# Kernel tuning notes

Hardware: AMD Instinct MI355X
Metric: run time of the kernel (lower is better)

## Reference

```python
import jax, jax.numpy as jnp
import numpy as np

B, T, D = 32, 2048, 512
BATCH_SIZE = 32  # config.batch_size: number of MVN draws


def setup_inputs() -> dict:
    key = jax.random.key(0)
    k1, k2 = jax.random.split(key)
    x = jax.random.normal(k1, (B, T, D), dtype=jnp.float32)
    z = jax.random.normal(k2, (BATCH_SIZE, D), dtype=jnp.float32)  # standard-normal noise for reparameterized MVN draw
    return {"x": x, "z": z}


def reference(x, z):
    # mean over batch and time -> [D]
    mean = jnp.mean(x, axis=(0, 1))
    # per-batch covariance over time axis, then mean over batch -> [D, D]
    t = x.shape[1]
    xc = x - jnp.mean(x, axis=1, keepdims=True)
    # sum over b and t fused: equals mean_b( xc_b^T xc_b / (t-1) )
    cov = jnp.einsum('btd,bte->de', xc, xc) / ((t - 1) * x.shape[0])
    # multivariate normal draw via Cholesky reparameterization:
    # sample = mean + z @ L^T, L L^T = cov
    L = jnp.linalg.cholesky(cov)
    return mean + z @ L.T
```

## Files before the change

kernel.cpp:

```cpp
#include <hip/hip_runtime.h>

#define Dn 512
#define Bn 32
#define Tn 2048
#define BT 65536

typedef unsigned short u16;
typedef __attribute__((ext_vector_type(8))) short short8;
typedef __attribute__((ext_vector_type(4))) float floatx4;

__device__ __forceinline__ u16 f2bf(float f) {
    unsigned u = __float_as_uint(f);
    unsigned r = (u + 0x7FFFu + ((u >> 16) & 1u)) >> 16;
    return (u16)r;
}
__device__ __forceinline__ float bf2f(u16 s) { return __uint_as_float(((unsigned)s) << 16); }

#define REP64(X) X(0) X(1) X(2) X(3) X(4) X(5) X(6) X(7) X(8) X(9) X(10) X(11) X(12) X(13) X(14) X(15) \
    X(16) X(17) X(18) X(19) X(20) X(21) X(22) X(23) X(24) X(25) X(26) X(27) X(28) X(29) X(30) X(31) \
    X(32) X(33) X(34) X(35) X(36) X(37) X(38) X(39) X(40) X(41) X(42) X(43) X(44) X(45) X(46) X(47) \
    X(48) X(49) X(50) X(51) X(52) X(53) X(54) X(55) X(56) X(57) X(58) X(59) X(60) X(61) X(62) X(63)
#define REPJ(OP, K) OP(K,0) OP(K,1) OP(K,2) OP(K,3) OP(K,4) OP(K,5) OP(K,6) OP(K,7) OP(K,8) OP(K,9) \
    OP(K,10) OP(K,11) OP(K,12) OP(K,13) OP(K,14) OP(K,15) OP(K,16) OP(K,17) OP(K,18) OP(K,19) \
    OP(K,20) OP(K,21) OP(K,22) OP(K,23) OP(K,24) OP(K,25) OP(K,26) OP(K,27) OP(K,28) OP(K,29) \
    OP(K,30) OP(K,31) OP(K,32) OP(K,33) OP(K,34) OP(K,35) OP(K,36) OP(K,37) OP(K,38) OP(K,39) \
    OP(K,40) OP(K,41) OP(K,42) OP(K,43) OP(K,44) OP(K,45) OP(K,46) OP(K,47) OP(K,48) OP(K,49) \
    OP(K,50) OP(K,51) OP(K,52) OP(K,53) OP(K,54) OP(K,55) OP(K,56) OP(K,57) OP(K,58) OP(K,59) \
    OP(K,60) OP(K,61) OP(K,62) OP(K,63)
#define REPQ(OP, C) OP(C,0,0,0) OP(C,1,0,1) OP(C,2,0,2) OP(C,3,0,3) OP(C,4,1,0) OP(C,5,1,1) OP(C,6,1,2) OP(C,7,1,3) \
    OP(C,8,2,0) OP(C,9,2,1) OP(C,10,2,2) OP(C,11,2,3) OP(C,12,3,0) OP(C,13,3,1) OP(C,14,3,2) OP(C,15,3,3) \
    OP(C,16,4,0) OP(C,17,4,1) OP(C,18,4,2) OP(C,19,4,3) OP(C,20,5,0) OP(C,21,5,1) OP(C,22,5,2) OP(C,23,5,3) \
    OP(C,24,6,0) OP(C,25,6,1) OP(C,26,6,2) OP(C,27,6,3) OP(C,28,7,0) OP(C,29,7,1) OP(C,30,7,2) OP(C,31,7,3) \
    OP(C,32,8,0) OP(C,33,8,1) OP(C,34,8,2) OP(C,35,8,3) OP(C,36,9,0) OP(C,37,9,1) OP(C,38,9,2) OP(C,39,9,3) \
    OP(C,40,10,0) OP(C,41,10,1) OP(C,42,10,2) OP(C,43,10,3) OP(C,44,11,0) OP(C,45,11,1) OP(C,46,11,2) OP(C,47,11,3) \
    OP(C,48,12,0) OP(C,49,12,1) OP(C,50,12,2) OP(C,51,12,3) OP(C,52,13,0) OP(C,53,13,1) OP(C,54,13,2) OP(C,55,13,3) \
    OP(C,56,14,0) OP(C,57,14,1) OP(C,58,14,2) OP(C,59,14,3) OP(C,60,15,0) OP(C,61,15,1) OP(C,62,15,2) OP(C,63,15,3)
#define REPW(OP) OP(0,0,1,2,3) OP(1,4,5,6,7) OP(2,8,9,10,11) OP(3,12,13,14,15) OP(4,16,17,18,19) \
    OP(5,20,21,22,23) OP(6,24,25,26,27) OP(7,28,29,30,31) OP(8,32,33,34,35) OP(9,36,37,38,39) \
    OP(10,40,41,42,43) OP(11,44,45,46,47) OP(12,48,49,50,51) OP(13,52,53,54,55) OP(14,56,57,58,59) \
    OP(15,60,61,62,63)
#define REP16C(OP, C) OP(C,0) OP(C,1) OP(C,2) OP(C,3) OP(C,4) OP(C,5) OP(C,6) OP(C,7) \
    OP(C,8) OP(C,9) OP(C,10) OP(C,11) OP(C,12) OP(C,13) OP(C,14) OP(C,15)

__global__ __launch_bounds__(256) void k_transpose(const float* __restrict__ x,
                                                   u16* __restrict__ Xt) {
    int tt = blockIdx.x;
    int dt = blockIdx.y;
    int b  = blockIdx.z;
    __shared__ u16 sT[64][68];
    int tid = threadIdx.x;
    int row = tid >> 4;
    int c4  = (tid & 15) * 4;
    const float* src = x + ((long)b * Tn + (long)tt * 64) * Dn + dt * 64;
#pragma unroll
    for (int q = 0; q < 4; q++) {
        int r = row + q * 16;
        floatx4 v = *(const floatx4*)(src + (long)r * Dn + c4);
        sT[c4 + 0][r] = f2bf(v[0]);
        sT[c4 + 1][r] = f2bf(v[1]);
        sT[c4 + 2][r] = f2bf(v[2]);
        sT[c4 + 3][r] = f2bf(v[3]);
    }
    __syncthreads();
    int drow = tid >> 3;
    int koff = (tid & 7) * 8;
    long kout = (long)b * Tn + (long)tt * 64 + koff;
#pragma unroll
    for (int p = 0; p < 2; p++) {
        int dr = drow + p * 32;
        u16 tmp[8];
#pragma unroll
        for (int j = 0; j < 8; j++) tmp[j] = sT[dr][koff + j];
        *(short8*)(Xt + (long)(dt * 64 + dr) * BT + kout) = *(short8*)tmp;
    }
}

__global__ __launch_bounds__(256) void k_mu(const u16* __restrict__ Xt,
                                            float* __restrict__ mu) {
    int tid = threadIdx.x;
    int wave = tid >> 6, lane = tid & 63;
    int p = blockIdx.x * 4 + wave;
    int b = p >> 9, d = p & 511;
    const u16* src = Xt + (long)d * BT + (long)b * Tn;
    float s = 0.f;
#pragma unroll
    for (int c = 0; c < 4; c++) {
        short8 v = *(const short8*)(src + c * 512 + lane * 8);
#pragma unroll
        for (int j = 0; j < 8; j++) s += bf2f((u16)v[j]);
    }
#pragma unroll
    for (int off = 32; off; off >>= 1) s += __shfl_down(s, off, 64);
    if (lane == 0) mu[p] = s * (1.0f / Tn);
}

#define LDK 40
__global__ __launch_bounds__(256) void k_gram(const u16* __restrict__ Xt,
                                              float* __restrict__ partial) {
    int chunk = blockIdx.x;
    int pos = blockIdx.y;
    int di = (pos < 4) ? 0 : (pos < 7) ? 1 : (pos < 9) ? 2 : 3;
    int start = di * 4 - (di * (di - 1)) / 2;
    int ei = di + (pos - start);
    int d0 = di * 128, e0 = ei * 128;

    __shared__ u16 sA[128 * LDK];
    __shared__ u16 sB[128 * LDK];
    int tid = threadIdx.x;
    int wave = tid >> 6, lane = tid & 63;
    int wm = wave & 1, wn = wave >> 1;
    int lrow = tid >> 2;
    int lk = (tid & 3) * 8;
    const u16* gA = Xt + (long)(d0 + lrow) * BT + (long)chunk * 4096 + lk;
    const u16* gB = Xt + (long)(e0 + lrow) * BT + (long)chunk * 4096 + lk;
    int m = lane & 15, g = lane >> 4;

    floatx4 acc[4][4] = {};
    for (int kk = 0; kk < 4096; kk += 32) {
        short8 a0 = *(const short8*)(gA + kk);
        short8 a1 = *(const short8*)(gA + 64l * BT + kk);
        short8 b0 = *(const short8*)(gB + kk);
        short8 b1 = *(const short8*)(gB + 64l * BT + kk);
        __syncthreads();
        *(short8*)(sA + lrow * LDK + lk) = a0;
        *(short8*)(sA + (lrow + 64) * LDK + lk) = a1;
        *(short8*)(sB + lrow * LDK + lk) = b0;
        *(short8*)(sB + (lrow + 64) * LDK + lk) = b1;
        __syncthreads();
        short8 af[4], bf[4];
#pragma unroll
        for (int i = 0; i < 4; i++)
            af[i] = *(const short8*)(sA + (wm * 64 + i * 16 + m) * LDK + g * 8);
#pragma unroll
        for (int j = 0; j < 4; j++)
            bf[j] = *(const short8*)(sB + (wn * 64 + j * 16 + m) * LDK + g * 8);
#pragma unroll
        for (int i = 0; i < 4; i++)
#pragma unroll
            for (int j = 0; j < 4; j++)
                acc[i][j] = __builtin_amdgcn_mfma_f32_16x16x32_bf16(af[i], bf[j], acc[i][j], 0, 0, 0);
    }
    float* P = partial + (long)chunk * (512l * 512);
    int col = lane & 15, rowg = (lane >> 4) * 4;
#pragma unroll
    for (int i = 0; i < 4; i++)
#pragma unroll
        for (int j = 0; j < 4; j++) {
            int rr = d0 + wm * 64 + i * 16 + rowg;
            int cc = e0 + wn * 64 + j * 16 + col;
#pragma unroll
            for (int r = 0; r < 4; r++) P[(long)(rr + r) * 512 + cc] = acc[i][j][r];
        }
}

__global__ __launch_bounds__(256) void k_assemble(const float* __restrict__ partial,
                                                  const float* __restrict__ mu,
                                                  float* __restrict__ A) {
    int d = blockIdx.y;
    int e = blockIdx.x * 256 + threadIdx.x;
    int bd = d >> 7, be = e >> 7;
    long idx = (bd <= be) ? ((long)d * 512 + e) : ((long)e * 512 + d);
    float s = 0.f;
#pragma unroll
    for (int c = 0; c < 16; c++) s += partial[c * (512l * 512) + idx];
    float msum = 0.f;
#pragma unroll
    for (int b = 0; b < 32; b++) msum += mu[b * 512 + d] * mu[b * 512 + e];
    A[(long)d * 512 + e] = (s - (float)Tn * msum) * (1.0f / ((Tn - 1.0f) * Bn));
}

__global__ __launch_bounds__(64, 1) void k_chol_panel(float* __restrict__ A, int kb) {
    const int k0 = kb * 64;
    const int lane = threadIdx.x;
    __shared__ float sD[64 * 68];
    __shared__ float sInv[64];
    const floatx4 z4 = {0.f, 0.f, 0.f, 0.f};

    const float* Dr = A + (long)(k0 + lane) * 512 + k0;
#define LDV(Q,A0,A1,A2,A3) floatx4 v##Q = *(const floatx4*)(Dr + 4*(Q));
    REPW(LDV)
#undef LDV
#define DECR(C,M,Mq,e) float r##M = v##Mq[(e)];
    REPQ(DECR, 0)
#undef DECR

    float vinv = 0.f;
#define SH1(K,J) float t##J = ((J) > (K)) ? __shfl(lik, (J), 64) : 0.0f;
#define FM1(K,J) if ((J) > (K)) r##J = fmaf(-lik, t##J, r##J);
#define STEP(K) { float akk = __shfl(r##K, (K), 64); float sd = sqrtf(akk); \
                  float inv = 1.0f / sd; float lik = (lane == (K)) ? sd : r##K * inv; \
                  r##K = lik; if (lane == (K)) vinv = inv; REPJ(SH1, K) REPJ(FM1, K) }
    REP64(STEP)
#undef STEP
#undef FM1
#undef SH1

    if (blockIdx.x == 0) {
        float* W = A + (long)(k0 + lane) * 512 + k0;
#define STW(Q,A0,A1,A2,A3) { floatx4 w; w[0]=r##A0; w[1]=r##A1; w[2]=r##A2; w[3]=r##A3; \
                             *(floatx4*)(W + 4*(Q)) = w; }
        REPW(STW)
#undef STW
        return;
    }

#define STD(Q,A0,A1,A2,A3) { floatx4 w; w[0]=r##A0; w[1]=r##A1; w[2]=r##A2; w[3]=r##A3; \
                             *(floatx4*)(sD + lane * 68 + 4*(Q)) = w; }
    REPW(STD)
#undef STD
    sInv[lane] = vinv;
    __syncthreads();

    int rbase = k0 + 64 + (blockIdx.x - 1) * 64;
    const float* R = A + (long)(rbase + lane) * 512 + k0;
#define LDA(Q,A0,A1,A2,A3) floatx4 u##Q = *(const floatx4*)(R + 4*(Q));
    REPW(LDA)
#undef LDA
#define DECA(C,M,Mq,e) float a##M = u##Mq[(e)];
    REPQ(DECA, 0)
#undef DECA
#define LQ(C,Q) floatx4 q##Q = ((C) > 4*(Q)) ? *(const floatx4*)(sD + (C) * 68 + 4*(Q)) : z4;
#define TF(C,M,Mq,e) if ((M) < (C)) acc##e = fmaf(a##M, q##Mq[(e)], acc##e);
#define TSTEP(C) { REP16C(LQ, C) float acc0 = 0.f, acc1 = 0.f, acc2 = 0.f, acc3 = 0.f; \
                   REPQ(TF, C) a##C = (a##C - ((acc0 + acc1) + (acc2 + acc3))) * sInv[(C)]; }
    REP64(TSTEP)
#undef TSTEP
#undef TF
#undef LQ

    float* Wr = A + (long)(rbase + lane) * 512 + k0;
#define STA(Q,A0,A1,A2,A3) { floatx4 w; w[0]=a##A0; w[1]=a##A1; w[2]=a##A2; w[3]=a##A3; \
                             *(floatx4*)(Wr + 4*(Q)) = w; }
    REPW(STA)
#undef STA
}

__global__ __launch_bounds__(256) void k_chol_update(float* __restrict__ A, int kb) {
    int k0 = kb * 64, base = k0 + 64;
    int idx = blockIdx.x, ti = 0;
    while (idx > ti) { idx -= ti + 1; ti++; }
    int tj = idx;
    int r0 = base + ti * 64, c0 = base + tj * 64;
    __shared__ float sI[64][65];
    __shared__ float sJ[64][65];
    int tid = threadIdx.x;
    int row = tid >> 4, c4 = (tid & 15) * 4;
#pragma unroll
    for (int q = 0; q < 4; q++) {
        int rr = row + q * 16;
        *(floatx4*)&sI[rr][c4] = *(const floatx4*)(A + (long)(r0 + rr) * 512 + k0 + c4);
        *(floatx4*)&sJ[rr][c4] = *(const floatx4*)(A + (long)(c0 + rr) * 512 + k0 + c4);
    }
    __syncthreads();
    int ri = (tid >> 4) * 4, cj = (tid & 15) * 4;
    float acc[4][4] = {};
    for (int k = 0; k < 64; k += 4) {
        floatx4 av[4], bv[4];
#pragma unroll
        for (int ii = 0; ii < 4; ii++) av[ii] = *(const floatx4*)&sI[ri + ii][k];
#pragma unroll
        for (int jj = 0; jj < 4; jj++) bv[jj] = *(const floatx4*)&sJ[cj + jj][k];
#pragma unroll
        for (int ii = 0; ii < 4; ii++)
#pragma unroll
            for (int jj = 0; jj < 4; jj++)
#pragma unroll
                for (int q = 0; q < 4; q++)
                    acc[ii][jj] = fmaf(av[ii][q], bv[jj][q], acc[ii][jj]);
    }
#pragma unroll
    for (int ii = 0; ii < 4; ii++) {
        float* dst = A + (long)(r0 + ri + ii) * 512 + c0 + cj;
        floatx4 old = *(const floatx4*)dst;
#pragma unroll
        for (int jj = 0; jj < 4; jj++) old[jj] -= acc[ii][jj];
        *(floatx4*)dst = old;
    }
}

__global__ __launch_bounds__(512) void k_output(const float* __restrict__ z,
                                                const float* __restrict__ A,
                                                const float* __restrict__ mu,
                                                float* __restrict__ out) {
    int i = blockIdx.x, d = threadIdx.x;
    __shared__ float sz[512];
    sz[d] = z[(long)i * 512 + d];
    __syncthreads();
    float mean = 0.f;
#pragma unroll
    for (int b = 0; b < 32; b++) mean += mu[b * 512 + d];
    mean *= (1.0f / 32.0f);
    const float* Lr = A + (long)d * 512;
    float acc = 0.f;
    int dmax = d + 1;
    int e4 = dmax & ~3;
    for (int e = 0; e < e4; e += 4) {
        floatx4 l = *(const floatx4*)(Lr + e);
        acc += l[0] * sz[e] + l[1] * sz[e + 1] + l[2] * sz[e + 2] + l[3] * sz[e + 3];
    }
    for (int e = e4; e < dmax; e++) acc += Lr[e] * sz[e];
    out[(long)i * 512 + d] = mean + acc;
}

extern "C" void kernel_launch(void* const* d_in, const int* in_sizes, int n_in,
                              void* d_out, int out_size, void* d_ws, size_t ws_size,
                              hipStream_t stream) {
    const float* x = (const float*)d_in[0];
    const float* z = (const float*)d_in[1];
    float* out = (float*)d_out;
    char* ws = (char*)d_ws;
    u16* Xt = (u16*)ws;
    float* mu = (float*)(ws + 67108864);
    float* partial = (float*)(ws + 67108864 + 65536);
    float* A = (float*)(ws + 67108864 + 65536 + 16777216);

    k_transpose<<<dim3(32, 8, 32), 256, 0, stream>>>(x, Xt);
    k_mu<<<4096, 256, 0, stream>>>(Xt, mu);
    k_gram<<<dim3(16, 10), 256, 0, stream>>>(Xt, partial);
    k_assemble<<<dim3(2, 512), 256, 0, stream>>>(partial, mu, A);
    for (int kb = 0; kb < 8; kb++) {
        int nb = 7 - kb;
        k_chol_panel<<<nb + 1, 64, 0, stream>>>(A, kb);
        int tiles = nb * (nb + 1) / 2;
        if (tiles > 0) k_chol_update<<<tiles, 256, 0, stream>>>(A, kb);
    }
    k_output<<<32, 512, 0, stream>>>(z, A, mu, out);
}
```

Before: 674.0 us.

## Split Gram into more chunks with direct LDS loads; switch Cholesky to left-looking

The Gram kernel now splits the time axis into 64 chunks instead of 16, giving 640 blocks rather than 160, and stages tiles with global_load_lds into unpadded shared memory. The assemble kernel sums 64 partials accordingly, and the partial buffer grows fourfold. The Cholesky is restructured from right-looking (a panel kernel plus a trailing-update kernel per step) into one left-looking kernel per step, which halves the number of launches. That kernel accumulates prior updates for its diagonal and sub-diagonal block before factorising. This trades redundant recomputation of the diagonal update in every block, plus extra partial-sum traffic, for better GPU occupancy and less launch overhead.

```diff
diff --git a/kernel.cpp b/kernel.cpp
--- a/kernel.cpp
+++ b/kernel.cpp
@@ -15,6 +15,10 @@
     return (u16)r;
 }
 __device__ __forceinline__ float bf2f(u16 s) { return __uint_as_float(((unsigned)s) << 16); }
+
+#define GLD16(gp, lp) __builtin_amdgcn_global_load_lds( \
+    (const __attribute__((address_space(1))) unsigned int*)(gp), \
+    (__attribute__((address_space(3))) unsigned int*)(lp), 16, 0, 0)
 
 #define REP64(X) X(0) X(1) X(2) X(3) X(4) X(5) X(6) X(7) X(8) X(9) X(10) X(11) X(12) X(13) X(14) X(15) \
     X(16) X(17) X(18) X(19) X(20) X(21) X(22) X(23) X(24) X(25) X(26) X(27) X(28) X(29) X(30) X(31) \
@@ -94,7 +98,6 @@
     if (lane == 0) mu[p] = s * (1.0f / Tn);
 }
 
-#define LDK 40
 __global__ __launch_bounds__(256) void k_gram(const u16* __restrict__ Xt,
                                               float* __restrict__ partial) {
     int chunk = blockIdx.x;
@@ -103,37 +106,35 @@
     int start = di * 4 - (di * (di - 1)) / 2;
     int ei = di + (pos - start);
     int d0 = di * 128, e0 = ei * 128;
-
-    __shared__ u16 sA[128 * LDK];
-    __shared__ u16 sB[128 * LDK];
+    long cb = (long)chunk << 10;
+
+    __shared__ u16 sA[128 * 32];
+    __shared__ u16 sB[128 * 32];
     int tid = threadIdx.x;
     int wave = tid >> 6, lane = tid & 63;
     int wm = wave & 1, wn = wave >> 1;
-    int lrow = tid >> 2;
-    int lk = (tid & 3) * 8;
-    const u16* gA = Xt + (long)(d0 + lrow) * BT + (long)chunk * 4096 + lk;
-    const u16* gB = Xt + (long)(e0 + lrow) * BT + (long)chunk * 4096 + lk;
     int m = lane & 15, g = lane >> 4;
 
+    const u16* gA0 = Xt + (long)(d0 + wave * 32 + (lane >> 2)) * BT + cb + (lane & 3) * 8;
+    const u16* gB0 = Xt + (long)(e0 + wave * 32 + (lane >> 2)) * BT + cb + (lane & 3) * 8;
+    u16* lA = sA + wave * 1024;
+    u16* lB = sB + wave * 1024;
+
     floatx4 acc[4][4] = {};
-    for (int kk = 0; kk < 4096; kk += 32) {
-        short8 a0 = *(const short8*)(gA + kk);
-        short8 a1 = *(const short8*)(gA + 64l * BT + kk);
-        short8 b0 = *(const short8*)(gB + kk);
-        short8 b1 = *(const short8*)(gB + 64l * BT + kk);
+    for (int kk = 0; kk < 1024; kk += 32) {
         __syncthreads();
-        *(short8*)(sA + lrow * LDK + lk) = a0;
-        *(short8*)(sA + (lrow + 64) * LDK + lk) = a1;
-        *(short8*)(sB + lrow * LDK + lk) = b0;
-        *(short8*)(sB + (lrow + 64) * LDK + lk) = b1;
+        GLD16(gA0 + kk, lA);
+        GLD16(gA0 + 16l * BT + kk, lA + 512);
+        GLD16(gB0 + kk, lB);
+        GLD16(gB0 + 16l * BT + kk, lB + 512);
         __syncthreads();
         short8 af[4], bf[4];
 #pragma unroll
         for (int i = 0; i < 4; i++)
-            af[i] = *(const short8*)(sA + (wm * 64 + i * 16 + m) * LDK + g * 8);
+            af[i] = *(const short8*)(sA + (wm * 64 + i * 16 + m) * 32 + g * 8);
 #pragma unroll
         for (int j = 0; j < 4; j++)
-            bf[j] = *(const short8*)(sB + (wn * 64 + j * 16 + m) * LDK + g * 8);
+            bf[j] = *(const short8*)(sB + (wn * 64 + j * 16 + m) * 32 + g * 8);
 #pragma unroll
         for (int i = 0; i < 4; i++)
 #pragma unroll
@@ -161,120 +162,129 @@
     int bd = d >> 7, be = e >> 7;
     long idx = (bd <= be) ? ((long)d * 512 + e) : ((long)e * 512 + d);
     float s = 0.f;
-#pragma unroll
-    for (int c = 0; c < 16; c++) s += partial[c * (512l * 512) + idx];
+#pragma unroll 8
+    for (int c = 0; c < 64; c++) s += partial[c * (512l * 512) + idx];
     float msum = 0.f;
 #pragma unroll
     for (int b = 0; b < 32; b++) msum += mu[b * 512 + d] * mu[b * 512 + e];
     A[(long)d * 512 + e] = (s - (float)Tn * msum) * (1.0f / ((Tn - 1.0f) * Bn));
 }
 
-__global__ __launch_bounds__(64, 1) void k_chol_panel(float* __restrict__ A, int kb) {
+__global__ __launch_bounds__(256, 1) void k_chol_left(float* __restrict__ A, int kb) {
     const int k0 = kb * 64;
-    const int lane = threadIdx.x;
+    const int bi = blockIdx.x;
+    const int r0 = k0 + bi * 64;
+    const int tid = threadIdx.x;
+    const int lane = tid & 63;
+    const int wv = tid >> 6;
+    __shared__ float sLd[64 * 65];
+    __shared__ float sLr[64 * 65];
     __shared__ float sD[64 * 68];
+    __shared__ float sS[64 * 68];
     __shared__ float sInv[64];
     const floatx4 z4 = {0.f, 0.f, 0.f, 0.f};
 
-    const float* Dr = A + (long)(k0 + lane) * 512 + k0;
+    int srow = tid >> 4, c4 = (tid & 15) * 4;
+    int ri = (tid >> 4) * 4, cj = (tid & 15) * 4;
+
+    floatx4 accD[4], accS[4];
+#pragma unroll
+    for (int ii = 0; ii < 4; ii++) {
+        accD[ii] = *(const floatx4*)(A + (long)(k0 + ri + ii) * 512 + k0 + cj);
+        accS[ii] = *(const floatx4*)(A + (long)(r0 + ri + ii) * 512 + k0 + cj);
+    }
+
+    for (int kc = 0; kc < k0; kc += 64) {
+        __syncthreads();
+#pragma unroll
+        for (int q = 0; q < 4; q++) {
+            int rr = srow + q * 16;
+            *(floatx4*)&sLd[rr * 65 + c4] = *(const floatx4*)(A + (long)(k0 + rr) * 512 + kc + c4);
+            *(floatx4*)&sLr[rr * 65 + c4] = *(const floatx4*)(A + (long)(r0 + rr) * 512 + kc + c4);
+        }
+        __syncthreads();
+        for (int k = 0; k < 64; k += 4) {
+            floatx4 ad[4], ar[4], bv[4];
+#pragma unroll
+            for (int ii = 0; ii < 4; ii++) ad[ii] = *(const floatx4*)&sLd[(ri + ii) * 65 + k];
+#pragma unroll
+            for (int ii = 0; ii < 4; ii++) ar[ii] = *(const floatx4*)&sLr[(ri + ii) * 65 + k];
+#pragma unroll
+            for (int jj = 0; jj < 4; jj++) bv[jj] = *(const floatx4*)&sLd[(cj + jj) * 65 + k];
+#pragma unroll
+            for (int ii = 0; ii < 4; ii++)
+#pragma unroll
+                for (int jj = 0; jj < 4; jj++)
+#pragma unroll
+                    for (int q = 0; q < 4; q++) {
+                        accD[ii][jj] = fmaf(-ad[ii][q], bv[jj][q], accD[ii][jj]);
+                        accS[ii][jj] = fmaf(-ar[ii][q], bv[jj][q], accS[ii][jj]);
+                    }
+        }
+    }
+
+#pragma unroll
+    for (int ii = 0; ii < 4; ii++) {
+        *(floatx4*)&sD[(ri + ii) * 68 + cj] = accD[ii];
+        *(floatx4*)&sS[(ri + ii) * 68 + cj] = accS[ii];
+    }
+    __syncthreads();
+
+    if (wv == 0) {
+        const float* Dr = sD + lane * 68;
 #define LDV(Q,A0,A1,A2,A3) floatx4 v##Q = *(const floatx4*)(Dr + 4*(Q));
-    REPW(LDV)
+        REPW(LDV)
 #undef LDV
 #define DECR(C,M,Mq,e) float r##M = v##Mq[(e)];
-    REPQ(DECR, 0)
+        REPQ(DECR, 0)
 #undef DECR
-
-    float vinv = 0.f;
+        float vinv = 0.f;
 #define SH1(K,J) float t##J = ((J) > (K)) ? __shfl(lik, (J), 64) : 0.0f;
 #define FM1(K,J) if ((J) > (K)) r##J = fmaf(-lik, t##J, r##J);
 #define STEP(K) { float akk = __shfl(r##K, (K), 64); float sd = sqrtf(akk); \
                   float inv = 1.0f / sd; float lik = (lane == (K)) ? sd : r##K * inv; \
                   r##K = lik; if (lane == (K)) vinv = inv; REPJ(SH1, K) REPJ(FM1, K) }
-    REP64(STEP)
+        REP64(STEP)
 #undef STEP
 #undef FM1
 #undef SH1
-
-    if (blockIdx.x == 0) {
-        float* W = A + (long)(k0 + lane) * 512 + k0;
+#define STD(Q,A0,A1,A2,A3) { floatx4 w; w[0]=r##A0; w[1]=r##A1; w[2]=r##A2; w[3]=r##A3; \
+                             *(floatx4*)(sD + lane * 68 + 4*(Q)) = w; }
+        REPW(STD)
+#undef STD
+        sInv[lane] = vinv;
+        if (bi == 0) {
+            float* W = A + (long)(k0 + lane) * 512 + k0;
 #define STW(Q,A0,A1,A2,A3) { floatx4 w; w[0]=r##A0; w[1]=r##A1; w[2]=r##A2; w[3]=r##A3; \
                              *(floatx4*)(W + 4*(Q)) = w; }
-        REPW(STW)
+            REPW(STW)
 #undef STW
-        return;
-    }
-
-#define STD(Q,A0,A1,A2,A3) { floatx4 w; w[0]=r##A0; w[1]=r##A1; w[2]=r##A2; w[3]=r##A3; \
-                             *(floatx4*)(sD + lane * 68 + 4*(Q)) = w; }
-    REPW(STD)
-#undef STD
-    sInv[lane] = vinv;
+        }
+    }
     __syncthreads();
-
-    int rbase = k0 + 64 + (blockIdx.x - 1) * 64;
-    const float* R = A + (long)(rbase + lane) * 512 + k0;
-#define LDA(Q,A0,A1,A2,A3) floatx4 u##Q = *(const floatx4*)(R + 4*(Q));
-    REPW(LDA)
+    if (bi == 0) return;
+
+    if (wv == 0) {
+        const float* Sr = sS + lane * 68;
+#define LDA(Q,A0,A1,A2,A3) floatx4 u##Q = *(const floatx4*)(Sr + 4*(Q));
+        REPW(LDA)
 #undef LDA
 #define DECA(C,M,Mq,e) float a##M = u##Mq[(e)];
-    REPQ(DECA, 0)
+        REPQ(DECA, 0)
 #undef DECA
 #define LQ(C,Q) floatx4 q##Q = ((C) > 4*(Q)) ? *(const floatx4*)(sD + (C) * 68 + 4*(Q)) : z4;
 #define TF(C,M,Mq,e) if ((M) < (C)) acc##e = fmaf(a##M, q##Mq[(e)], acc##e);
 #define TSTEP(C) { REP16C(LQ, C) float acc0 = 0.f, acc1 = 0.f, acc2 = 0.f, acc3 = 0.f; \
                    REPQ(TF, C) a##C = (a##C - ((acc0 + acc1) + (acc2 + acc3))) * sInv[(C)]; }
-    REP64(TSTEP)
+        REP64(TSTEP)
 #undef TSTEP
 #undef TF
 #undef LQ
-
-    float* Wr = A + (long)(rbase + lane) * 512 + k0;
+        float* Wr = A + (long)(r0 + lane) * 512 + k0;
 #define STA(Q,A0,A1,A2,A3) { floatx4 w; w[0]=a##A0; w[1]=a##A1; w[2]=a##A2; w[3]=a##A3; \
                              *(floatx4*)(Wr + 4*(Q)) = w; }
-    REPW(STA)
+        REPW(STA)
 #undef STA
-}
-
-__global__ __launch_bounds__(256) void k_chol_update(float* __restrict__ A, int kb) {
-    int k0 = kb * 64, base = k0 + 64;
-    int idx = blockIdx.x, ti = 0;
-    while (idx > ti) { idx -= ti + 1; ti++; }
-    int tj = idx;
-    int r0 = base + ti * 64, c0 = base + tj * 64;
-    __shared__ float sI[64][65];
-    __shared__ float sJ[64][65];
-    int tid = threadIdx.x;
-    int row = tid >> 4, c4 = (tid & 15) * 4;
-#pragma unroll
-    for (int q = 0; q < 4; q++) {
-        int rr = row + q * 16;
-        *(floatx4*)&sI[rr][c4] = *(const floatx4*)(A + (long)(r0 + rr) * 512 + k0 + c4);
-        *(floatx4*)&sJ[rr][c4] = *(const floatx4*)(A + (long)(c0 + rr) * 512 + k0 + c4);
-    }
-    __syncthreads();
-    int ri = (tid >> 4) * 4, cj = (tid & 15) * 4;
-    float acc[4][4] = {};
-    for (int k = 0; k < 64; k += 4) {
-        floatx4 av[4], bv[4];
-#pragma unroll
-        for (int ii = 0; ii < 4; ii++) av[ii] = *(const floatx4*)&sI[ri + ii][k];
-#pragma unroll
-        for (int jj = 0; jj < 4; jj++) bv[jj] = *(const floatx4*)&sJ[cj + jj][k];
-#pragma unroll
-        for (int ii = 0; ii < 4; ii++)
-#pragma unroll
-            for (int jj = 0; jj < 4; jj++)
-#pragma unroll
-                for (int q = 0; q < 4; q++)
-                    acc[ii][jj] = fmaf(av[ii][q], bv[jj][q], acc[ii][jj]);
-    }
-#pragma unroll
-    for (int ii = 0; ii < 4; ii++) {
-        float* dst = A + (long)(r0 + ri + ii) * 512 + c0 + cj;
-        floatx4 old = *(const floatx4*)dst;
-#pragma unroll
-        for (int jj = 0; jj < 4; jj++) old[jj] -= acc[ii][jj];
-        *(floatx4*)dst = old;
     }
 }
 
@@ -312,17 +322,13 @@
     u16* Xt = (u16*)ws;
     float* mu = (float*)(ws + 67108864);
     float* partial = (float*)(ws + 67108864 + 65536);
-    float* A = (float*)(ws + 67108864 + 65536 + 16777216);
+    float* A = (float*)(ws + 67108864 + 65536 + 67108864);
 
     k_transpose<<<dim3(32, 8, 32), 256, 0, stream>>>(x, Xt);
     k_mu<<<4096, 256, 0, stream>>>(Xt, mu);
-    k_gram<<<dim3(16, 10), 256, 0, stream>>>(Xt, partial);
+    k_gram<<<dim3(64, 10), 256, 0, stream>>>(Xt, partial);
     k_assemble<<<dim3(2, 512), 256, 0, stream>>>(partial, mu, A);
-    for (int kb = 0; kb < 8; kb++) {
-        int nb = 7 - kb;
-        k_chol_panel<<<nb + 1, 64, 0, stream>>>(A, kb);
-        int tiles = nb * (nb + 1) / 2;
-        if (tiles > 0) k_chol_update<<<tiles, 256, 0, stream>>>(A, kb);
-    }
+    for (int kb = 0; kb < 8; kb++)
+        k_chol_left<<<8 - kb, 256, 0, stream>>>(A, kb);
     k_output<<<32, 512, 0, stream>>>(z, A, mu, out);
 }
```

Measured after the change: 744.7 us. 1.1x slower.
